# Kernel optimization log

Hardware: AMD Instinct MI355X
Metric: run time of the kernel (lower is better)

## Reference

```python
import jax, jax.numpy as jnp
import numpy as np

S = 4  # search_range_spatial -> 9 spatial shifts per axis
D = 1  # search_range_depth   -> 3 depth shifts


def setup_inputs() -> dict:
    key = jax.random.key(0)
    k1, k2, k3, k4 = jax.random.split(key, 4)
    b, c, h, w, d = 4, 64, 96, 96, 8
    return {
        "mpi1_features": jax.random.normal(k1, (b, c, h, w, d), dtype=jnp.float32),
        "mpi1_alpha": jax.random.uniform(k2, (b, 1, h, w, d), dtype=jnp.float32),
        "mpi2_features": jax.random.normal(k3, (b, c, h, w, d), dtype=jnp.float32),
        "mpi2_alpha": jax.random.uniform(k4, (b, 1, h, w, d), dtype=jnp.float32),
    }


def reference(mpi1_features, mpi1_alpha, mpi2_features, mpi2_alpha):
    b, c, h, w, d = mpi1_features.shape
    # visibility masks: any alpha along depth, clipped to [0,1]
    mask1 = jnp.clip(jnp.sum(mpi1_alpha, axis=-1, keepdims=True), 0.0, 1.0)
    mask2 = jnp.clip(jnp.sum(mpi2_alpha, axis=-1, keepdims=True), 0.0, 1.0)
    mask1 = jnp.broadcast_to(mask1, mpi1_alpha.shape)
    mask2 = jnp.broadcast_to(mask2, mpi2_alpha.shape)
    # pad second MPI: zeros for features, ones for mask (matches torch F.pad values)
    pad = ((0, 0), (0, 0), (S, S), (S, S), (D, D))
    f2 = jnp.pad(mpi2_features, pad, mode="constant", constant_values=0.0)
    m2 = jnp.pad(mask2, pad, mode="constant", constant_values=1.0)
    cv, cvm = [], []
    for k in range(2 * D + 1):
        for i in range(2 * S + 1):
            for j in range(2 * S + 1):
                f2s = f2[:, :, i:i + h, j:j + w, k:k + d]
                m2s = m2[:, :, i:i + h, j:j + w, k:k + d]
                cost = jnp.mean(mpi1_features * f2s, axis=1, keepdims=True)
                cost_mask = jnp.clip(
                    jnp.sum(mask1 * m2s, axis=1, keepdims=True), 0.0, 1.0)
                cv.append(cost)
                cvm.append(cost_mask)
    cost_volume = jnp.concatenate(cv, axis=1)       # [b, 243, h, w, d]
    cost_volume_mask = jnp.concatenate(cvm, axis=1)  # [b, 243, h, w, d]
    return cost_volume, cost_volume_mask
```

## Files before the change

kernel.cpp:

```cpp
#include <hip/hip_runtime.h>

#define BB 4
#define CH 64
#define HH 96
#define WW 96
#define DD 8
#define NS 243
#define CC 2

__global__ void masks_kernel(const float* __restrict__ a1,
                             const float* __restrict__ a2,
                             float* __restrict__ m1,
                             float* __restrict__ m2) {
    int p = blockIdx.x * 256 + threadIdx.x;
    if (p >= BB * HH * WW) return;
    float4 x0 = ((const float4*)a1)[p * 2];
    float4 x1 = ((const float4*)a1)[p * 2 + 1];
    float4 y0 = ((const float4*)a2)[p * 2];
    float4 y1 = ((const float4*)a2)[p * 2 + 1];
    float s1 = ((x0.x + x0.y) + (x0.z + x0.w)) + ((x1.x + x1.y) + (x1.z + x1.w));
    float s2 = ((y0.x + y0.y) + (y0.z + y0.w)) + ((y1.x + y1.y) + (y1.z + y1.w));
    m1[p] = fminf(fmaxf(s1, 0.0f), 1.0f);
    m2[p] = fminf(fmaxf(s2, 0.0f), 1.0f);
}

__global__ __launch_bounds__(256)
void maskvol_kernel(const float* __restrict__ m1,
                    const float* __restrict__ m2,
                    float* __restrict__ out) {
    int bs = blockIdx.x;
    int q  = blockIdx.y;
    int b = bs / NS;
    int s = bs % NS;
    int k = s / 81;
    int i = (s / 9) % 9;
    int j = s % 9;
    const float* m1b = m1 + b * HH * WW;
    const float* m2b = m2 + b * HH * WW;
    float4* o4 = (float4*)out + (size_t)bs * (HH * WW * DD / 4);
    int n_end = (q + 1) * 4608;
    for (int n = q * 4608 + threadIdx.x; n < n_end; n += 256) {
        int y = n / 192;
        int r = n - y * 192;
        int x = r >> 1;
        int zb = (r & 1) * 4;
        float m1v = m1b[y * WW + x];
        int yy = y + i - 4;
        int xx = x + j - 4;
        float m2v = 1.0f;
        if ((unsigned)yy < HH && (unsigned)xx < WW) m2v = m2b[yy * WW + xx];
        float pv = m1v * m2v;
        float4 v;
        float* vp = (float*)&v;
        #pragma unroll
        for (int t = 0; t < 4; ++t) {
            int zz = zb + t + k - 1;
            float r0 = ((unsigned)zz < DD) ? pv : m1v;
            vp[t] = fminf(fmaxf(r0, 0.0f), 1.0f);
        }
        o4[n] = v;
    }
}

__global__ __launch_bounds__(192, 3)
void cost_kernel(const float* __restrict__ f1,
                 const float* __restrict__ f2,
                 float* __restrict__ out) {
    const int L = blockIdx.x;
    const int u = L % 216;
    const int t9 = u >> 3;
    const int i = t9 % 9;
    const int k = t9 / 9;
    const int g = (L / 216) * 8 + (u & 7);
    const int b = g / HH;
    const int y = g % HH;
    const int tid = threadIdx.x;
    const int xb = tid >> 3;
    const int z  = tid & 7;
    const int yp = y + i - 4;

    if (yp < 0 || yp >= HH) {
        #pragma unroll
        for (int j = 0; j < 9; ++j) {
            int s = k * 81 + i * 9 + j;
            float4* o4 = (float4*)out + ((size_t)(b * NS + s) * HH + y) * 192;
            o4[tid] = make_float4(0.f, 0.f, 0.f, 0.f);
        }
        return;
    }

    __shared__ __align__(16) float smem[CC * 8 * 96 + CC * 10 * 104];
    float (*f1s)[8][96]   = (float (*)[8][96])smem;
    float (*f2s)[10][104] = (float (*)[10][104])(smem + CC * 8 * 96);

    for (int n = tid; n < CC * 10 * 104; n += 192)
        ((float*)f2s)[n] = 0.0f;

    const int xs = tid >> 1;
    const int zb = (tid & 1) * 4;

    const float4* f1r = (const float4*)f1 + ((size_t)(b * CH) * HH + y)  * 192;
    const float4* f2r = (const float4*)f2 + ((size_t)(b * CH) * HH + yp) * 192;

    float4 p1[CC], p2[CC];
    #pragma unroll
    for (int c = 0; c < CC; ++c) {
        p1[c] = f1r[(size_t)c * (HH * 192) + tid];
        p2[c] = f2r[(size_t)c * (HH * 192) + tid];
    }

    float acc[9][4];
    #pragma unroll
    for (int j = 0; j < 9; ++j)
        #pragma unroll
        for (int t = 0; t < 4; ++t)
            acc[j][t] = 0.0f;

    for (int c0 = 0; c0 < CH; c0 += CC) {
        __syncthreads();
        #pragma unroll
        for (int c = 0; c < CC; ++c) {
            f1s[c][zb + 0][xs] = p1[c].x;
            f1s[c][zb + 1][xs] = p1[c].y;
            f1s[c][zb + 2][xs] = p1[c].z;
            f1s[c][zb + 3][xs] = p1[c].w;
            f2s[c][zb + 1][xs + 4] = p2[c].x;
            f2s[c][zb + 2][xs + 4] = p2[c].y;
            f2s[c][zb + 3][xs + 4] = p2[c].z;
            f2s[c][zb + 4][xs + 4] = p2[c].w;
        }
        __syncthreads();
        if (c0 + CC < CH) {
            #pragma unroll
            for (int c = 0; c < CC; ++c) {
                p1[c] = f1r[(size_t)(c0 + CC + c) * (HH * 192) + tid];
                p2[c] = f2r[(size_t)(c0 + CC + c) * (HH * 192) + tid];
            }
        }

        #pragma unroll
        for (int c = 0; c < CC; ++c) {
            float4 f1v = *(const float4*)&f1s[c][z][xb * 4];
            float f1a[4] = {f1v.x, f1v.y, f1v.z, f1v.w};
            float4 w0 = *(const float4*)&f2s[c][z + k][xb * 4];
            float4 w1 = *(const float4*)&f2s[c][z + k][xb * 4 + 4];
            float4 w2 = *(const float4*)&f2s[c][z + k][xb * 4 + 8];
            float w[12] = {w0.x, w0.y, w0.z, w0.w,
                           w1.x, w1.y, w1.z, w1.w,
                           w2.x, w2.y, w2.z, w2.w};
            #pragma unroll
            for (int t = 0; t < 4; ++t)
                #pragma unroll
                for (int j = 0; j < 9; ++j)
                    acc[j][t] = fmaf(f1a[t], w[t + j], acc[j][t]);
        }
    }

    __syncthreads();
    float* sbuf = smem;
    int wsw[4];
    #pragma unroll
    for (int t = 0; t < 4; ++t) {
        int d  = (xb * 4 + t) * 8 + z;
        int bb = d >> 2;
        int sb = bb ^ ((bb >> 3) & 7);
        wsw[t] = (sb << 2) | (d & 3);
    }
    const int rsw = (tid ^ ((tid >> 3) & 7)) << 2;

    #pragma unroll
    for (int jb = 0; jb < 3; ++jb) {
        #pragma unroll
        for (int jj = 0; jj < 3; ++jj)
            #pragma unroll
            for (int t = 0; t < 4; ++t)
                sbuf[jj * 768 + wsw[t]] = acc[jb * 3 + jj][t] * 0.015625f;
        __syncthreads();
        #pragma unroll
        for (int jj = 0; jj < 3; ++jj) {
            int s = k * 81 + i * 9 + jb * 3 + jj;
            float4 v = *(float4*)&sbuf[jj * 768 + rsw];
            float4* o4 = (float4*)out + ((size_t)(b * NS + s) * HH + y) * 192;
            o4[tid] = v;
        }
        __syncthreads();
    }
}

extern "C" void kernel_launch(void* const* d_in, const int* in_sizes, int n_in,
                              void* d_out, int out_size, void* d_ws, size_t ws_size,
                              hipStream_t stream) {
    const float* f1 = (const float*)d_in[0];
    const float* a1 = (const float*)d_in[1];
    const float* f2 = (const float*)d_in[2];
    const float* a2 = (const float*)d_in[3];

    float* out      = (float*)d_out;
    float* out_cost = out;
    float* out_mask = out + (size_t)BB * NS * HH * WW * DD;

    float* m1 = (float*)d_ws;
    float* m2 = m1 + BB * HH * WW;

    masks_kernel<<<(BB * HH * WW + 255) / 256, 256, 0, stream>>>(a1, a2, m1, m2);
    maskvol_kernel<<<dim3(BB * NS, 4), 256, 0, stream>>>(m1, m2, out_mask);
    cost_kernel<<<10368, 192, 0, stream>>>(f1, f2, out_cost);
}
```

Measured before the change: 845.8 us.

## Fuse mask-volume writes into cost kernel and read f1 directly from global

Removes the separate mask-volume kernel and writes the mask output from the cost kernel's epilogue, using row indices it already has. This saves a launch and lets the two output streams share one pass. Feature map f1 is no longer staged in shared memory. Each thread reads its four f1 values per channel straight from global memory with strided scalar loads, which cuts LDS footprint and LDS stores. The f2 staging also changes to a new thread mapping. The risk is uncoalesced scalar global loads for f1 and f2 and extra work in the epilogue. Clipping of the mask product is dropped, which is valid because both inputs are already in [0,1].

```diff
diff --git a/kernel.cpp b/kernel.cpp
--- a/kernel.cpp
+++ b/kernel.cpp
@@ -7,6 +7,7 @@
 #define DD 8
 #define NS 243
 #define CC 2
+#define CSTRIDE (HH * WW * DD)
 
 __global__ void masks_kernel(const float* __restrict__ a1,
                              const float* __restrict__ a2,
@@ -24,48 +25,13 @@
     m2[p] = fminf(fmaxf(s2, 0.0f), 1.0f);
 }
 
-__global__ __launch_bounds__(256)
-void maskvol_kernel(const float* __restrict__ m1,
-                    const float* __restrict__ m2,
-                    float* __restrict__ out) {
-    int bs = blockIdx.x;
-    int q  = blockIdx.y;
-    int b = bs / NS;
-    int s = bs % NS;
-    int k = s / 81;
-    int i = (s / 9) % 9;
-    int j = s % 9;
-    const float* m1b = m1 + b * HH * WW;
-    const float* m2b = m2 + b * HH * WW;
-    float4* o4 = (float4*)out + (size_t)bs * (HH * WW * DD / 4);
-    int n_end = (q + 1) * 4608;
-    for (int n = q * 4608 + threadIdx.x; n < n_end; n += 256) {
-        int y = n / 192;
-        int r = n - y * 192;
-        int x = r >> 1;
-        int zb = (r & 1) * 4;
-        float m1v = m1b[y * WW + x];
-        int yy = y + i - 4;
-        int xx = x + j - 4;
-        float m2v = 1.0f;
-        if ((unsigned)yy < HH && (unsigned)xx < WW) m2v = m2b[yy * WW + xx];
-        float pv = m1v * m2v;
-        float4 v;
-        float* vp = (float*)&v;
-        #pragma unroll
-        for (int t = 0; t < 4; ++t) {
-            int zz = zb + t + k - 1;
-            float r0 = ((unsigned)zz < DD) ? pv : m1v;
-            vp[t] = fminf(fmaxf(r0, 0.0f), 1.0f);
-        }
-        o4[n] = v;
-    }
-}
-
 __global__ __launch_bounds__(192, 3)
 void cost_kernel(const float* __restrict__ f1,
                  const float* __restrict__ f2,
-                 float* __restrict__ out) {
+                 const float* __restrict__ m1,
+                 const float* __restrict__ m2,
+                 float* __restrict__ outc,
+                 float* __restrict__ outm) {
     const int L = blockIdx.x;
     const int u = L % 216;
     const int t9 = u >> 3;
@@ -79,35 +45,42 @@
     const int z  = tid & 7;
     const int yp = y + i - 4;
 
+    const int ex  = tid >> 1;
+    const int ezb = (tid & 1) * 4;
+    const float m1v = m1[(b * HH + y) * WW + ex];
+
     if (yp < 0 || yp >= HH) {
+        float4 mv = make_float4(m1v, m1v, m1v, m1v);
         #pragma unroll
         for (int j = 0; j < 9; ++j) {
             int s = k * 81 + i * 9 + j;
-            float4* o4 = (float4*)out + ((size_t)(b * NS + s) * HH + y) * 192;
-            o4[tid] = make_float4(0.f, 0.f, 0.f, 0.f);
+            size_t ro = ((size_t)(b * NS + s) * HH + y) * 192;
+            ((float4*)outc)[ro + tid] = make_float4(0.f, 0.f, 0.f, 0.f);
+            ((float4*)outm)[ro + tid] = mv;
         }
         return;
     }
 
-    __shared__ __align__(16) float smem[CC * 8 * 96 + CC * 10 * 104];
-    float (*f1s)[8][96]   = (float (*)[8][96])smem;
-    float (*f2s)[10][104] = (float (*)[10][104])(smem + CC * 8 * 96);
+    __shared__ __align__(16) float smem[2304];
+    float* f2s = smem;
 
-    for (int n = tid; n < CC * 10 * 104; n += 192)
-        ((float*)f2s)[n] = 0.0f;
+    for (int n = tid; n < CC * 1040; n += 192) f2s[n] = 0.0f;
 
-    const int xs = tid >> 1;
-    const int zb = (tid & 1) * 4;
+    const int sx = tid % 24;
+    const int sz = tid / 24;
 
-    const float4* f1r = (const float4*)f1 + ((size_t)(b * CH) * HH + y)  * 192;
-    const float4* f2r = (const float4*)f2 + ((size_t)(b * CH) * HH + yp) * 192;
+    const float* f1g = f1 + ((size_t)(b * CH) * HH + y ) * (WW * DD);
+    const float* f2g = f2 + ((size_t)(b * CH) * HH + yp) * (WW * DD);
+    const int f2off = (sx * 4) * 8 + sz;
+    const int f1off = (xb * 4) * 8 + z;
+    const int sdst  = (sz + 1) * 104 + sx * 4 + 4;
 
-    float4 p1[CC], p2[CC];
+    float pf[CC][4];
     #pragma unroll
-    for (int c = 0; c < CC; ++c) {
-        p1[c] = f1r[(size_t)c * (HH * 192) + tid];
-        p2[c] = f2r[(size_t)c * (HH * 192) + tid];
-    }
+    for (int c = 0; c < CC; ++c)
+        #pragma unroll
+        for (int t = 0; t < 4; ++t)
+            pf[c][t] = f2g[(size_t)c * CSTRIDE + f2off + t * 8];
 
     float acc[9][4];
     #pragma unroll
@@ -120,31 +93,29 @@
         __syncthreads();
         #pragma unroll
         for (int c = 0; c < CC; ++c) {
-            f1s[c][zb + 0][xs] = p1[c].x;
-            f1s[c][zb + 1][xs] = p1[c].y;
-            f1s[c][zb + 2][xs] = p1[c].z;
-            f1s[c][zb + 3][xs] = p1[c].w;
-            f2s[c][zb + 1][xs + 4] = p2[c].x;
-            f2s[c][zb + 2][xs + 4] = p2[c].y;
-            f2s[c][zb + 3][xs + 4] = p2[c].z;
-            f2s[c][zb + 4][xs + 4] = p2[c].w;
+            float4 v;
+            v.x = pf[c][0]; v.y = pf[c][1]; v.z = pf[c][2]; v.w = pf[c][3];
+            *(float4*)&f2s[c * 1040 + sdst] = v;
         }
         __syncthreads();
         if (c0 + CC < CH) {
             #pragma unroll
-            for (int c = 0; c < CC; ++c) {
-                p1[c] = f1r[(size_t)(c0 + CC + c) * (HH * 192) + tid];
-                p2[c] = f2r[(size_t)(c0 + CC + c) * (HH * 192) + tid];
-            }
+            for (int c = 0; c < CC; ++c)
+                #pragma unroll
+                for (int t = 0; t < 4; ++t)
+                    pf[c][t] = f2g[(size_t)(c0 + CC + c) * CSTRIDE + f2off + t * 8];
         }
 
         #pragma unroll
         for (int c = 0; c < CC; ++c) {
-            float4 f1v = *(const float4*)&f1s[c][z][xb * 4];
-            float f1a[4] = {f1v.x, f1v.y, f1v.z, f1v.w};
-            float4 w0 = *(const float4*)&f2s[c][z + k][xb * 4];
-            float4 w1 = *(const float4*)&f2s[c][z + k][xb * 4 + 4];
-            float4 w2 = *(const float4*)&f2s[c][z + k][xb * 4 + 8];
+            float f1a[4];
+            #pragma unroll
+            for (int t = 0; t < 4; ++t)
+                f1a[t] = f1g[(size_t)(c0 + c) * CSTRIDE + f1off + t * 8];
+            const float* wp = &f2s[c * 1040 + (z + k) * 104 + xb * 4];
+            float4 w0 = *(const float4*)(wp);
+            float4 w1 = *(const float4*)(wp + 4);
+            float4 w2 = *(const float4*)(wp + 8);
             float w[12] = {w0.x, w0.y, w0.z, w0.w,
                            w1.x, w1.y, w1.z, w1.w,
                            w2.x, w2.y, w2.z, w2.w};
@@ -168,6 +139,8 @@
     }
     const int rsw = (tid ^ ((tid >> 3) & 7)) << 2;
 
+    const float* m2b = m2 + (b * HH + yp) * WW;
+
     #pragma unroll
     for (int jb = 0; jb < 3; ++jb) {
         #pragma unroll
@@ -178,10 +151,22 @@
         __syncthreads();
         #pragma unroll
         for (int jj = 0; jj < 3; ++jj) {
-            int s = k * 81 + i * 9 + jb * 3 + jj;
+            int j = jb * 3 + jj;
+            int s = k * 81 + i * 9 + j;
+            size_t ro = ((size_t)(b * NS + s) * HH + y) * 192;
             float4 v = *(float4*)&sbuf[jj * 768 + rsw];
-            float4* o4 = (float4*)out + ((size_t)(b * NS + s) * HH + y) * 192;
-            o4[tid] = v;
+            ((float4*)outc)[ro + tid] = v;
+            int xp = ex + j - 4;
+            float m2v = ((unsigned)xp < WW) ? m2b[xp] : 1.0f;
+            float pv = m1v * m2v;
+            float4 mv;
+            float* mp = (float*)&mv;
+            #pragma unroll
+            for (int q = 0; q < 4; ++q) {
+                int zz = ezb + q + k - 1;
+                mp[q] = ((unsigned)zz < DD) ? pv : m1v;
+            }
+            ((float4*)outm)[ro + tid] = mv;
         }
         __syncthreads();
     }
@@ -203,6 +188,5 @@
     float* m2 = m1 + BB * HH * WW;
 
     masks_kernel<<<(BB * HH * WW + 255) / 256, 256, 0, stream>>>(a1, a2, m1, m2);
-    maskvol_kernel<<<dim3(BB * NS, 4), 256, 0, stream>>>(m1, m2, out_mask);
-    cost_kernel<<<10368, 192, 0, stream>>>(f1, f2, out_cost);
+    cost_kernel<<<10368, 192, 0, stream>>>(f1, f2, m1, m2, out_cost, out_mask);
 }
```

Measured after the change: 1.501 ms. 77.5% more time.
